# Performance work log

Hardware: AMD Instinct MI355X
Metric: run time of the kernel (lower is better)

The kernel has to match this reference:

```python
import jax, jax.numpy as jnp
import numpy as np

B, S, E, H, W = 4, 2048, 1024, 16, 512  # batch, seq, embed, heads, sliding window
D = E // H
NB = S // W  # number of query blocks
SCALE = 1.0 / np.sqrt(D)  # flex_attention default scale applied BEFORE score_mod
START_TOKEN = 0


def setup_inputs() -> dict:
    key = jax.random.key(0)
    k1, k2, k3 = jax.random.split(key, 3)
    x = jax.random.normal(k1, (B, S, E), jnp.float32)
    w_in = jax.random.normal(k2, (3 * E, E), jnp.float32) * 0.02   # packed qkv, Linear(E,3E,bias=False)
    w_out = jax.random.normal(k3, (E, E), jnp.float32) * 0.02      # Linear(E,E,bias=False)
    return {"x": x, "w_in": w_in, "w_out": w_out}


def _attn(x, w_in, w_out):
    # packed in-projection: proj.unflatten(-1,(3,E)) -> q,k,v
    proj = x @ w_in.T                                   # [B,S,3E]
    q, k, v = jnp.split(proj, 3, axis=-1)
    to_heads = lambda t: t.reshape(B, S, H, D).transpose(0, 2, 1, 3)  # [B,H,S,D]
    q, k, v = to_heads(q), to_heads(k), to_heads(v)

    # honor sliding-window sparsity: each query block of size W attends only
    # to its own block and the previous block (q_idx>=kv_idx & q_idx-kv_idx<W)
    qb = q.reshape(B, H, NB, W, D)
    kb = k.reshape(B, H, NB, W, D)
    vb = v.reshape(B, H, NB, W, D)
    pad = jnp.zeros((B, H, 1, W, D), q.dtype)
    k2 = jnp.concatenate([jnp.concatenate([pad, kb[:, :, :-1]], axis=2), kb], axis=3)  # [B,H,NB,2W,D]
    v2 = jnp.concatenate([jnp.concatenate([pad, vb[:, :, :-1]], axis=2), vb], axis=3)

    scores = jnp.einsum('bhnqd,bhnkd->bhnqk', qb, k2) * SCALE        # [B,H,NB,W,2W]

    # relative position q_idx - kv_idx (same for every block by construction)
    qi = jnp.arange(W)[:, None]
    ki = jnp.arange(2 * W)[None, :]
    rel = qi + W - ki                                                # [W,2W]

    # ALiBi: score + (q_idx + start_token - kv_idx) * exp2(-(h+1)*8/H)  (code ADDS bias)
    slopes = jnp.exp2(-(jnp.arange(1, H + 1, dtype=jnp.float32) * 8.0 / H))  # [H]
    bias = (rel.astype(jnp.float32) + START_TOKEN)[None, :, :] * slopes[:, None, None]  # [H,W,2W]
    scores = scores + bias[None, :, None, :, :]

    # causal + sliding window mask, and invalidate the zero-padded block before block 0
    win_mask = (rel >= 0) & (rel < W)                                # [W,2W]
    blk = jnp.arange(NB)[:, None, None]
    kv_valid = (blk >= 1) | (ki[None, :, :] >= W)                    # [NB,1,2W]
    mask = win_mask[None, :, :] & kv_valid                           # [NB,W,2W]
    scores = jnp.where(mask[None, None], scores, -jnp.inf)

    p = jax.nn.softmax(scores, axis=-1)
    o = jnp.einsum('bhnqk,bhnkd->bhnqd', p, v2).reshape(B, H, S, D)
    o = o.transpose(0, 2, 1, 3).reshape(B, S, E)
    return o @ w_out.T                                               # [B,S,E]


def reference(x, w_in, w_out):
    return _attn(x, w_in, w_out)
```

## Files before the change

kernel.cpp:

```cpp
#include <hip/hip_runtime.h>

typedef unsigned short ushort_t;
typedef __attribute__((ext_vector_type(8))) __bf16 bf16x8;
typedef __attribute__((ext_vector_type(4))) float f32x4;

#define EXP2F(x) __builtin_amdgcn_exp2f(x)
#define LOG2E 1.44269504088896340736f


__device__ __forceinline__ ushort_t f2bf(float f) {
  unsigned u = __float_as_uint(f);
  u += 0x7fffu + ((u >> 16) & 1u);
  return (ushort_t)(u >> 16);
}

__device__ __forceinline__ f32x4 mfma16(bf16x8 a, bf16x8 b, f32x4 c) {
  return __builtin_amdgcn_mfma_f32_16x16x32_bf16(a, b, c, 0, 0, 0);
}

__device__ __forceinline__ void gload16(const ushort_t* g, ushort_t* l) {
  __builtin_amdgcn_global_load_lds((__attribute__((address_space(1))) void*)g,
                                   (__attribute__((address_space(3))) void*)l,
                                   16, 0, 0);
}

__global__ __launch_bounds__(256) void cast_two(const float* __restrict__ a,
                                                ushort_t* __restrict__ oa, int na,
                                                const float* __restrict__ b,
                                                ushort_t* __restrict__ ob, int nb) {
  int i = (blockIdx.x * 256 + threadIdx.x) * 4;
  if (i < na) {
    float4 v = *(const float4*)(a + i);
    ushort4 o;
    o.x = f2bf(v.x); o.y = f2bf(v.y); o.z = f2bf(v.z); o.w = f2bf(v.w);
    *(ushort4*)(oa + i) = o;
  } else {
    int j = i - na;
    if (j < nb) {
      float4 v = *(const float4*)(b + j);
      ushort4 o;
      o.x = f2bf(v.x); o.y = f2bf(v.y); o.z = f2bf(v.z); o.w = f2bf(v.w);
      *(ushort4*)(ob + j) = o;
    }
  }
}

__global__ __launch_bounds__(256) void cast_f32_bf16(const float* __restrict__ in,
                                                     ushort_t* __restrict__ out, int n) {
  int i = (blockIdx.x * 256 + threadIdx.x) * 4;
  if (i < n) {
    float4 v = *(const float4*)(in + i);
    ushort4 o;
    o.x = f2bf(v.x); o.y = f2bf(v.y); o.z = f2bf(v.z); o.w = f2bf(v.w);
    *(ushort4*)(out + i) = o;
  }
}

template <bool C_F32, bool FUSE_V>
__global__ __launch_bounds__(256) void gemm_bt(const ushort_t* __restrict__ A,
                                               const ushort_t* __restrict__ Bt,
                                               void* __restrict__ Cp,
                                               ushort_t* __restrict__ Vt,
                                               int N, int K, int ldA) {
  __shared__ ushort_t As[128 * 64];
  __shared__ ushort_t Bs[128 * 64];
  const int tid = threadIdx.x;
  const int wave = tid >> 6;
  const int lane = tid & 63;
  const int g = lane >> 4;
  const int q = lane & 15;
  const int qm = q & 7;
  const int row0 = blockIdx.y * 128;
  const int col0 = blockIdx.x * 128;
  const int wm = (wave >> 1) * 64;
  const int wn = (wave & 1) * 64;

  const f32x4 fzero = {0.f, 0.f, 0.f, 0.f};
  f32x4 acc[4][4];
#pragma unroll
  for (int i = 0; i < 4; ++i)
#pragma unroll
    for (int j = 0; j < 4; ++j) acc[i][j] = fzero;

  const int rs = tid >> 3;
  const int cs = (((tid & 7) ^ (rs & 7)) << 3);
  const ushort_t* ag = A + (size_t)(row0 + rs) * ldA + cs;
  const ushort_t* bg = Bt + (size_t)(col0 + rs) * K + cs;
  ushort_t* lA = As + (size_t)(wave * 64 + lane) * 8;
  ushort_t* lB = Bs + (size_t)(wave * 64 + lane) * 8;

  const int sw0 = ((g ^ qm) << 3);
  const int sw1 = (((4 + g) ^ qm) << 3);

  for (int kt = 0; kt < K; kt += 64) {
    __syncthreads();
#pragma unroll
    for (int u = 0; u < 4; ++u) {
      gload16(ag + (size_t)(u * 32) * ldA + kt, lA + u * 2048);
      gload16(bg + (size_t)(u * 32) * K + kt, lB + u * 2048);
    }
    __syncthreads();
#pragma unroll
    for (int ks = 0; ks < 2; ++ks) {
      const int sw = ks ? sw1 : sw0;
      bf16x8 af[4], bfv[4];
#pragma unroll
      for (int mi = 0; mi < 4; ++mi)
        af[mi] = *(const bf16x8*)(As + (wm + mi * 16 + q) * 64 + sw);
#pragma unroll
      for (int ni = 0; ni < 4; ++ni)
        bfv[ni] = *(const bf16x8*)(Bs + (wn + ni * 16 + q) * 64 + sw);
      __builtin_amdgcn_s_setprio(1);
#pragma unroll
      for (int mi = 0; mi < 4; ++mi)
#pragma unroll
        for (int ni = 0; ni < 4; ++ni)
          acc[mi][ni] = mfma16(af[mi], bfv[ni], acc[mi][ni]);
      __builtin_amdgcn_s_setprio(0);
    }
  }

  if (FUSE_V && col0 >= 2048) {
#pragma unroll
    for (int mi = 0; mi < 4; ++mi) {
      const int rr = row0 + wm + mi * 16 + 4 * g;
      const int bb = rr >> 11;
      const int pbase = ((rr & 2047) & ~31) + 8 * g + 4 * (mi & 1);
#pragma unroll
      for (int ni = 0; ni < 4; ++ni) {
        const int cc = col0 + wn + ni * 16 + q - 2048;
        const int bh = bb * 16 + (cc >> 6);
        const int dd = cc & 63;
        ushort4 o;
        o.x = f2bf(acc[mi][ni][0]); o.y = f2bf(acc[mi][ni][1]);
        o.z = f2bf(acc[mi][ni][2]); o.w = f2bf(acc[mi][ni][3]);
        *(ushort4*)(Vt + (size_t)(bh * 64 + dd) * 2048 + pbase) = o;
      }
    }
  } else {
#pragma unroll
    for (int mi = 0; mi < 4; ++mi)
#pragma unroll
      for (int ni = 0; ni < 4; ++ni)
#pragma unroll
        for (int r = 0; r < 4; ++r) {
          size_t rr = (size_t)(row0 + wm + mi * 16 + 4 * g + r);
          size_t cc = (size_t)(col0 + wn + ni * 16 + q);
          if (C_F32) ((float*)Cp)[rr * N + cc] = acc[mi][ni][r];
          else ((ushort_t*)Cp)[rr * N + cc] = f2bf(acc[mi][ni][r]);
        }
  }
}

__global__ __launch_bounds__(512, 4) void attn_kernel(const ushort_t* __restrict__ proj,
                                                      const ushort_t* __restrict__ Vt,
                                                      ushort_t* __restrict__ attn_out,
                                                      int ostride) {
  __shared__ ushort_t Ks[2][4096];
  __shared__ ushort_t Vs[2][4096];
  const int tid = threadIdx.x;
  const int wave = tid >> 6;
  const int lane = tid & 63;
  const int g = lane >> 4;
  const int q = lane & 15;
  const int bid = blockIdx.x;
  const int xcd = bid & 7;
  const int j = bid >> 3;
  const int bh = xcd * 8 + (j >> 4);
  const int tile = j & 15;
  const int b = bh >> 4;
  const int h = bh & 15;
  const int q0b = tile * 128;
  const int qw0 = q0b + wave * 16;
  const int qglob = qw0 + q;

  const float slope2 = EXP2F(-(float)(h + 1) * 0.5f) * LOG2E;
  const float sc2 = 0.125f * LOG2E;

  const ushort_t* qptr = proj + (size_t)(b * 2048 + qglob) * 3072 + h * 64 + g * 8;
  const bf16x8 qa0 = *(const bf16x8*)(qptr);
  const bf16x8 qa1 = *(const bf16x8*)(qptr + 32);

  const int r0 = tid >> 3;
  const int c0s = (((tid & 7) ^ (r0 & 7)) << 3);
  const ushort_t* kgb = proj + (size_t)(b * 2048) * 3072 + 1024 + h * 64;
  const ushort_t* vgb = Vt + (size_t)(bh * 64) * 2048;

  const int qm = q & 7;
  const int sw0 = ((g ^ qm) << 3);
  const int sw1 = (((g + 4) ^ qm) << 3);

  const f32x4 fzero = {0.f, 0.f, 0.f, 0.f};
  f32x4 acc[4];
#pragma unroll
  for (int t2 = 0; t2 < 4; ++t2) acc[t2] = fzero;
  float m2 = -1e30f;
  float lsum = 0.f;
  const int relbase = qglob - 4 * g;

  int kc_lo = q0b - 512;
  if (kc_lo < 0) kc_lo = 0;
  const int nch = ((q0b + 127 - kc_lo) >> 6) + 1;

#define STAGE(bi, kcv)                                                        \
  gload16(kgb + (size_t)((kcv) + r0) * 3072 + c0s, &Ks[bi][(size_t)tid * 8]); \
  gload16(vgb + (size_t)r0 * 2048 + (kcv) + c0s, &Vs[bi][(size_t)tid * 8]);

  STAGE(0, kc_lo)
  __syncthreads();

  for (int c = 0; c < nch; ++c) {
    const int kc = kc_lo + (c << 6);
    const ushort_t* Kb = Ks[c & 1];
    const ushort_t* Vb = Vs[c & 1];
    if (c + 1 < nch) { STAGE((c + 1) & 1, kc + 64) }

    if (kc <= qw0 + 15 && kc >= qw0 - 574) {
      const int rbi = relbase - kc;
      float p[16];
      float mc = -1e30f;

      if (kc >= qw0 - 496 && kc <= qw0 - 63) {
        const float bb = (float)rbi * slope2;
        __builtin_amdgcn_s_setprio(1);
#pragma unroll
        for (int i = 0; i < 4; ++i) {
          const int row = (i << 4) + q;
          bf16x8 ka = *(const bf16x8*)(Kb + row * 64 + sw0);
          bf16x8 kb = *(const bf16x8*)(Kb + row * 64 + sw1);
          f32x4 si = mfma16(kb, qa1, mfma16(ka, qa0, fzero));
#pragma unroll
          for (int r = 0; r < 4; ++r) {
            float sc = fmaf(si[r], sc2, bb) - (float)((i << 4) + r) * slope2;
            p[(i << 2) + r] = sc;
            mc = fmaxf(mc, sc);
          }
        }
        __builtin_amdgcn_s_setprio(0);
      } else {
        __builtin_amdgcn_s_setprio(1);
#pragma unroll
        for (int i = 0; i < 4; ++i) {
          const int row = (i << 4) + q;
          bf16x8 ka = *(const bf16x8*)(Kb + row * 64 + sw0);
          bf16x8 kb = *(const bf16x8*)(Kb + row * 64 + sw1);
          f32x4 si = mfma16(kb, qa1, mfma16(ka, qa0, fzero));
#pragma unroll
          for (int r = 0; r < 4; ++r) {
            const int rel = rbi - ((i << 4) + r);
            float sc = ((unsigned)rel < 512u) ? fmaf(si[r], sc2, (float)rel * slope2)
                                              : -1e30f;
            p[(i << 2) + r] = sc;
            mc = fmaxf(mc, sc);
          }
        }
        __builtin_amdgcn_s_setprio(0);
      }

      if (__any(mc > m2 + 8.f)) {
        float mg = fmaxf(mc, m2);
        mg = fmaxf(mg, __shfl_xor(mg, 16, 64));
        mg = fmaxf(mg, __shfl_xor(mg, 32, 64));
        const float factor = EXP2F(m2 - mg);
        lsum *= factor;
#pragma unroll
        for (int t2 = 0; t2 < 4; ++t2) acc[t2] *= factor;
        m2 = mg;
      }
#pragma unroll
      for (int i = 0; i < 16; ++i) p[i] = EXP2F(p[i] - m2);
      float ps0 = (p[0] + p[1]) + (p[2] + p[3]);
      float ps1 = (p[4] + p[5]) + (p[6] + p[7]);
      float ps2 = (p[8] + p[9]) + (p[10] + p[11]);
      float ps3 = (p[12] + p[13]) + (p[14] + p[15]);
      lsum += (ps0 + ps1) + (ps2 + ps3);

      bf16x8 pv0, pv1;
#pragma unroll
      for (int r = 0; r < 4; ++r) {
        pv0[r] = (__bf16)p[r];       pv0[4 + r] = (__bf16)p[4 + r];
        pv1[r] = (__bf16)p[8 + r];   pv1[4 + r] = (__bf16)p[12 + r];
      }

      __builtin_amdgcn_s_setprio(1);
#pragma unroll
      for (int t2 = 0; t2 < 4; ++t2) {
        const int d = (t2 << 4) + q;
        bf16x8 vf0 = *(const bf16x8*)(Vb + d * 64 + sw0);
        bf16x8 vf1 = *(const bf16x8*)(Vb + d * 64 + sw1);
        acc[t2] = mfma16(vf0, pv0, acc[t2]);
        acc[t2] = mfma16(vf1, pv1, acc[t2]);
      }
      __builtin_amdgcn_s_setprio(0);
    }

    __syncthreads();
  }
#undef STAGE

  lsum += __shfl_xor(lsum, 16, 64);
  lsum += __shfl_xor(lsum, 32, 64);
  const float inv = 1.f / lsum;

  ushort_t* ob = attn_out + (size_t)(b * 2048 + qglob) * ostride + h * 64;
#pragma unroll
  for (int t2 = 0; t2 < 4; ++t2)
#pragma unroll
    for (int r = 0; r < 4; ++r)
      ob[16 * t2 + 4 * g + r] = f2bf(acc[t2][r] * inv);
}

extern "C" void kernel_launch(void* const* d_in, const int* in_sizes, int n_in,
                              void* d_out, int out_size, void* d_ws, size_t ws_size,
                              hipStream_t stream) {
  const float* x = nullptr;
  const float* w_in = nullptr;
  const float* w_out = nullptr;
  for (int i = 0; i < n_in; ++i) {
    if (in_sizes[i] == 8388608) x = (const float*)d_in[i];
    else if (in_sizes[i] == 3145728) w_in = (const float*)d_in[i];
    else if (in_sizes[i] == 1048576) w_out = (const float*)d_in[i];
  }
  if (!(x && w_in && w_out)) { x = (const float*)d_in[0]; w_in = (const float*)d_in[1]; w_out = (const float*)d_in[2]; }

  char* ws = (char*)d_ws;
  ushort_t* proj = (ushort_t*)(ws);
  ushort_t* xb   = (ushort_t*)(ws + (size_t)50331648);
  ushort_t* wob  = xb;
  ushort_t* wib  = (ushort_t*)d_out;
  ushort_t* Vt   = (ushort_t*)((char*)d_out + (size_t)8388608);

  cast_two<<<11264, 256, 0, stream>>>(x, xb, 8388608, w_in, wib, 3145728);
  gemm_bt<false, true><<<dim3(24, 64), 256, 0, stream>>>(xb, wib, proj, Vt, 3072, 1024, 1024);
  cast_f32_bf16<<<1024, 256, 0, stream>>>(w_out, wob, 1048576);
  attn_kernel<<<1024, 512, 0, stream>>>(proj, Vt, proj + 2048, 3072);
  gemm_bt<true, false><<<dim3(8, 64), 256, 0, stream>>>(proj + 2048, wob, d_out, nullptr, 1024, 1024, 3072);
}
```

Baseline: 138.6 us.

## Double-buffer GEMM LDS tiles with BK=32 to overlap loads and MFMA

Replaces the single 128x64 LDS tile and its two barriers per K step with two 128x32 buffers. The next K slice is prefetched via global_load_lds while MFMAs run on the current one, leaving one barrier per iteration. This aims to hide global load latency behind compute. In exchange the K step is halved, so there are twice as many iterations and barriers, less MFMA work per barrier, and a new 4-way XOR swizzle.

```diff
diff --git a/kernel.cpp b/kernel.cpp
--- a/kernel.cpp
+++ b/kernel.cpp
@@ -62,14 +62,13 @@
                                                void* __restrict__ Cp,
                                                ushort_t* __restrict__ Vt,
                                                int N, int K, int ldA) {
-  __shared__ ushort_t As[128 * 64];
-  __shared__ ushort_t Bs[128 * 64];
+  __shared__ ushort_t As[2][128 * 32];
+  __shared__ ushort_t Bs[2][128 * 32];
   const int tid = threadIdx.x;
   const int wave = tid >> 6;
   const int lane = tid & 63;
   const int g = lane >> 4;
   const int q = lane & 15;
-  const int qm = q & 7;
   const int row0 = blockIdx.y * 128;
   const int col0 = blockIdx.x * 128;
   const int wm = (wave >> 1) * 64;
@@ -82,43 +81,47 @@
 #pragma unroll
     for (int j = 0; j < 4; ++j) acc[i][j] = fzero;
 
-  const int rs = tid >> 3;
-  const int cs = (((tid & 7) ^ (rs & 7)) << 3);
+  const int rs = tid >> 2;
+  const int cs = (((tid & 3) ^ (rs & 3)) << 3);
   const ushort_t* ag = A + (size_t)(row0 + rs) * ldA + cs;
   const ushort_t* bg = Bt + (size_t)(col0 + rs) * K + cs;
-  ushort_t* lA = As + (size_t)(wave * 64 + lane) * 8;
-  ushort_t* lB = Bs + (size_t)(wave * 64 + lane) * 8;
-
-  const int sw0 = ((g ^ qm) << 3);
-  const int sw1 = (((4 + g) ^ qm) << 3);
-
-  for (int kt = 0; kt < K; kt += 64) {
+  const int ldst = tid * 8;
+
+  const int swr = ((g ^ (q & 3)) << 3);
+
+#define GSTAGE(bi, kt)                                                   \
+  {                                                                      \
+    gload16(ag + (kt), &As[bi][ldst]);                                   \
+    gload16(ag + (size_t)64 * ldA + (kt), &As[bi][ldst + 2048]);         \
+    gload16(bg + (kt), &Bs[bi][ldst]);                                   \
+    gload16(bg + (size_t)64 * K + (kt), &Bs[bi][ldst + 2048]);           \
+  }
+
+  GSTAGE(0, 0)
+  __syncthreads();
+  int cur = 0;
+  for (int kt = 0; kt < K; kt += 32) {
+    if (kt + 32 < K) { GSTAGE(cur ^ 1, kt + 32) }
+    const ushort_t* Ab = As[cur];
+    const ushort_t* Bb = Bs[cur];
+    bf16x8 af[4], bfv[4];
+#pragma unroll
+    for (int mi = 0; mi < 4; ++mi)
+      af[mi] = *(const bf16x8*)(Ab + (wm + mi * 16 + q) * 32 + swr);
+#pragma unroll
+    for (int ni = 0; ni < 4; ++ni)
+      bfv[ni] = *(const bf16x8*)(Bb + (wn + ni * 16 + q) * 32 + swr);
+    __builtin_amdgcn_s_setprio(1);
+#pragma unroll
+    for (int mi = 0; mi < 4; ++mi)
+#pragma unroll
+      for (int ni = 0; ni < 4; ++ni)
+        acc[mi][ni] = mfma16(af[mi], bfv[ni], acc[mi][ni]);
+    __builtin_amdgcn_s_setprio(0);
     __syncthreads();
-#pragma unroll
-    for (int u = 0; u < 4; ++u) {
-      gload16(ag + (size_t)(u * 32) * ldA + kt, lA + u * 2048);
-      gload16(bg + (size_t)(u * 32) * K + kt, lB + u * 2048);
-    }
-    __syncthreads();
-#pragma unroll
-    for (int ks = 0; ks < 2; ++ks) {
-      const int sw = ks ? sw1 : sw0;
-      bf16x8 af[4], bfv[4];
-#pragma unroll
-      for (int mi = 0; mi < 4; ++mi)
-        af[mi] = *(const bf16x8*)(As + (wm + mi * 16 + q) * 64 + sw);
-#pragma unroll
-      for (int ni = 0; ni < 4; ++ni)
-        bfv[ni] = *(const bf16x8*)(Bs + (wn + ni * 16 + q) * 64 + sw);
-      __builtin_amdgcn_s_setprio(1);
-#pragma unroll
-      for (int mi = 0; mi < 4; ++mi)
-#pragma unroll
-        for (int ni = 0; ni < 4; ++ni)
-          acc[mi][ni] = mfma16(af[mi], bfv[ni], acc[mi][ni]);
-      __builtin_amdgcn_s_setprio(0);
-    }
-  }
+    cur ^= 1;
+  }
+#undef GSTAGE
 
   if (FUSE_V && col0 >= 2048) {
 #pragma unroll
```

After: 151.4 us. 9.3% more time.

## Triple-buffer GEMM loads with 8-wave 128x256 tiles and split barriers

Applied to the files above, without the earlier changes.

The GEMM now uses 512-thread blocks with 128x256 output tiles and a three-stage LDS ring buffer. Global-to-LDS loads for tile t+2 are issued while tile t is computed, with explicit vmcnt waits and barriers in place of the old load-then-sync loop. The goal is to hide global memory latency and reuse each A tile across more columns. The cost is three times the LDS footprint, which may limit occupancy, and fewer blocks for the smaller output GEMM (256 blocks).

```diff
diff --git a/kernel.cpp b/kernel.cpp
--- a/kernel.cpp
+++ b/kernel.cpp
@@ -57,23 +57,23 @@
 }
 
 template <bool C_F32, bool FUSE_V>
-__global__ __launch_bounds__(256) void gemm_bt(const ushort_t* __restrict__ A,
-                                               const ushort_t* __restrict__ Bt,
-                                               void* __restrict__ Cp,
-                                               ushort_t* __restrict__ Vt,
-                                               int N, int K, int ldA) {
-  __shared__ ushort_t As[128 * 64];
-  __shared__ ushort_t Bs[128 * 64];
+__global__ __launch_bounds__(512, 2) void gemm_bt(const ushort_t* __restrict__ A,
+                                                  const ushort_t* __restrict__ Bt,
+                                                  void* __restrict__ Cp,
+                                                  ushort_t* __restrict__ Vt,
+                                                  int N, int K, int ldA) {
+  __shared__ ushort_t As[3][128 * 64];
+  __shared__ ushort_t Bs[3][256 * 64];
   const int tid = threadIdx.x;
   const int wave = tid >> 6;
   const int lane = tid & 63;
   const int g = lane >> 4;
   const int q = lane & 15;
   const int qm = q & 7;
+  const int wr = wave >> 2;
+  const int wc = wave & 3;
   const int row0 = blockIdx.y * 128;
-  const int col0 = blockIdx.x * 128;
-  const int wm = (wave >> 1) * 64;
-  const int wn = (wave & 1) * 64;
+  const int col0 = blockIdx.x * 256;
 
   const f32x4 fzero = {0.f, 0.f, 0.f, 0.f};
   f32x4 acc[4][4];
@@ -86,30 +86,42 @@
   const int cs = (((tid & 7) ^ (rs & 7)) << 3);
   const ushort_t* ag = A + (size_t)(row0 + rs) * ldA + cs;
   const ushort_t* bg = Bt + (size_t)(col0 + rs) * K + cs;
-  ushort_t* lA = As + (size_t)(wave * 64 + lane) * 8;
-  ushort_t* lB = Bs + (size_t)(wave * 64 + lane) * 8;
+  const int ld8 = tid * 8;
 
   const int sw0 = ((g ^ qm) << 3);
   const int sw1 = (((4 + g) ^ qm) << 3);
 
-  for (int kt = 0; kt < K; kt += 64) {
-    __syncthreads();
-#pragma unroll
-    for (int u = 0; u < 4; ++u) {
-      gload16(ag + (size_t)(u * 32) * ldA + kt, lA + u * 2048);
-      gload16(bg + (size_t)(u * 32) * K + kt, lB + u * 2048);
-    }
-    __syncthreads();
-#pragma unroll
-    for (int ks = 0; ks < 2; ++ks) {
-      const int sw = ks ? sw1 : sw0;
+#define STAGE6(bi, kt) {                                            \
+    gload16(ag + (kt), &As[bi][ld8]);                               \
+    gload16(ag + (size_t)64 * ldA + (kt), &As[bi][4096 + ld8]);     \
+    gload16(bg + (kt), &Bs[bi][ld8]);                               \
+    gload16(bg + (size_t)64 * K + (kt), &Bs[bi][4096 + ld8]);       \
+    gload16(bg + (size_t)128 * K + (kt), &Bs[bi][8192 + ld8]);      \
+    gload16(bg + (size_t)192 * K + (kt), &Bs[bi][12288 + ld8]);     \
+  }
+
+  const int nt = K >> 6;
+  STAGE6(0, 0)
+  STAGE6(1, 64)
+  asm volatile("s_waitcnt vmcnt(6)" ::: "memory");
+  __builtin_amdgcn_s_barrier();
+
+  for (int t = 0; t < nt; ++t) {
+    const int kt = t << 6;
+    const int cur = t % 3;
+    const ushort_t* Ab = As[cur] + (wr * 64 + q) * 64;
+    const ushort_t* Bb = Bs[cur] + (wc * 64 + q) * 64;
+
+    {
       bf16x8 af[4], bfv[4];
 #pragma unroll
       for (int mi = 0; mi < 4; ++mi)
-        af[mi] = *(const bf16x8*)(As + (wm + mi * 16 + q) * 64 + sw);
+        af[mi] = *(const bf16x8*)(Ab + mi * 1024 + sw0);
 #pragma unroll
       for (int ni = 0; ni < 4; ++ni)
-        bfv[ni] = *(const bf16x8*)(Bs + (wn + ni * 16 + q) * 64 + sw);
+        bfv[ni] = *(const bf16x8*)(Bb + ni * 1024 + sw0);
+      if (t + 2 < nt) { const int nb = (t + 2) % 3; STAGE6(nb, kt + 128) }
+      __builtin_amdgcn_s_barrier();
       __builtin_amdgcn_s_setprio(1);
 #pragma unroll
       for (int mi = 0; mi < 4; ++mi)
@@ -117,18 +129,41 @@
         for (int ni = 0; ni < 4; ++ni)
           acc[mi][ni] = mfma16(af[mi], bfv[ni], acc[mi][ni]);
       __builtin_amdgcn_s_setprio(0);
-    }
-  }
+      __builtin_amdgcn_s_barrier();
+    }
+
+    {
+      bf16x8 af[4], bfv[4];
+#pragma unroll
+      for (int mi = 0; mi < 4; ++mi)
+        af[mi] = *(const bf16x8*)(Ab + mi * 1024 + sw1);
+#pragma unroll
+      for (int ni = 0; ni < 4; ++ni)
+        bfv[ni] = *(const bf16x8*)(Bb + ni * 1024 + sw1);
+      if (t + 2 < nt) asm volatile("s_waitcnt vmcnt(6)" ::: "memory");
+      else            asm volatile("s_waitcnt vmcnt(0)" ::: "memory");
+      __builtin_amdgcn_s_barrier();
+      __builtin_amdgcn_s_setprio(1);
+#pragma unroll
+      for (int mi = 0; mi < 4; ++mi)
+#pragma unroll
+        for (int ni = 0; ni < 4; ++ni)
+          acc[mi][ni] = mfma16(af[mi], bfv[ni], acc[mi][ni]);
+      __builtin_amdgcn_s_setprio(0);
+      __builtin_amdgcn_s_barrier();
+    }
+  }
+#undef STAGE6
 
   if (FUSE_V && col0 >= 2048) {
 #pragma unroll
     for (int mi = 0; mi < 4; ++mi) {
-      const int rr = row0 + wm + mi * 16 + 4 * g;
+      const int rr = row0 + wr * 64 + mi * 16 + 4 * g;
       const int bb = rr >> 11;
       const int pbase = ((rr & 2047) & ~31) + 8 * g + 4 * (mi & 1);
 #pragma unroll
       for (int ni = 0; ni < 4; ++ni) {
-        const int cc = col0 + wn + ni * 16 + q - 2048;
+        const int cc = col0 + wc * 64 + ni * 16 + q - 2048;
         const int bh = bb * 16 + (cc >> 6);
         const int dd = cc & 63;
         ushort4 o;
@@ -144,8 +179,8 @@
       for (int ni = 0; ni < 4; ++ni)
 #pragma unroll
         for (int r = 0; r < 4; ++r) {
-          size_t rr = (size_t)(row0 + wm + mi * 16 + 4 * g + r);
-          size_t cc = (size_t)(col0 + wn + ni * 16 + q);
+          size_t rr = (size_t)(row0 + wr * 64 + mi * 16 + 4 * g + r);
+          size_t cc = (size_t)(col0 + wc * 64 + ni * 16 + q);
           if (C_F32) ((float*)Cp)[rr * N + cc] = acc[mi][ni][r];
           else ((ushort_t*)Cp)[rr * N + cc] = f2bf(acc[mi][ni][r]);
         }
@@ -331,8 +366,8 @@
   ushort_t* Vt   = (ushort_t*)((char*)d_out + (size_t)8388608);
 
   cast_two<<<11264, 256, 0, stream>>>(x, xb, 8388608, w_in, wib, 3145728);
-  gemm_bt<false, true><<<dim3(24, 64), 256, 0, stream>>>(xb, wib, proj, Vt, 3072, 1024, 1024);
+  gemm_bt<false, true><<<dim3(12, 64), 512, 0, stream>>>(xb, wib, proj, Vt, 3072, 1024, 1024);
   cast_f32_bf16<<<1024, 256, 0, stream>>>(w_out, wob, 1048576);
   attn_kernel<<<1024, 512, 0, stream>>>(proj, Vt, proj + 2048, 3072);
-  gemm_bt<true, false><<<dim3(8, 64), 256, 0, stream>>>(proj + 2048, wob, d_out, nullptr, 1024, 1024, 3072);
-}
+  gemm_bt<true, false><<<dim3(4, 64), 512, 0, stream>>>(proj + 2048, wob, d_out, nullptr, 1024, 1024, 3072);
+}
```

Result: slower. 157.1 us (+13.4%).
